# Kernel optimization log

Measured on AMD Instinct MI355X. Metric: run time of the kernel, lower is better.

## Reference

```python
import jax, jax.numpy as jnp
import numpy as np

B, S, D, H = 8, 1024, 1024, 16
HD = D // H  # head_dim = 64


def setup_inputs() -> dict:
    key = jax.random.key(0)
    ks = jax.random.split(key, 5)
    scale = 1.0 / np.sqrt(D)
    return {
        "x": jax.random.normal(ks[0], (B, S, D), dtype=jnp.float32),
        "wq": jax.random.normal(ks[1], (D, D), dtype=jnp.float32) * scale,
        "wk": jax.random.normal(ks[2], (D, D), dtype=jnp.float32) * scale,
        "wv": jax.random.normal(ks[3], (D, D), dtype=jnp.float32) * scale,
        "wo": jax.random.normal(ks[4], (D, D), dtype=jnp.float32) * scale,
    }


def reference(x, wq, wk, wv, wo):
    b, s, d = x.shape
    # nn.Linear: y = x @ W.T  (weights stored [out, in])
    q = (x @ wq.T).reshape(b, s, H, HD).transpose(0, 2, 1, 3)  # [b,h,s,hd]
    k = (x @ wk.T).reshape(b, s, H, HD).transpose(0, 2, 1, 3)
    v = (x @ wv.T).reshape(b, s, H, HD).transpose(0, 2, 1, 3)
    scores = jnp.einsum("bhqd,bhkd->bhqk", q, k) / jnp.sqrt(jnp.float32(HD))
    attn = jax.nn.softmax(scores, axis=-1)  # dropout p=0.0 -> identity
    out = jnp.einsum("bhqk,bhkd->bhqd", attn, v)
    out = out.transpose(0, 2, 1, 3).reshape(b, s, d)
    return out @ wo.T
```

## Files before the change

kernel.cpp:

```cpp
#include <hip/hip_runtime.h>
#include <hip/hip_bf16.h>
#include <math.h>

#define BB 8
#define SS 1024
#define DD 1024
#define HH 16
#define HDIM 64
#define MM (BB * SS)
#define QSCALE 0.1803368801111204f

typedef __attribute__((ext_vector_type(8))) short s8v;
typedef __attribute__((ext_vector_type(4))) short s4v;
typedef __attribute__((ext_vector_type(4))) float f4v;

#define GLD16(g, l)                                                            \
  __builtin_amdgcn_global_load_lds(                                            \
      (const __attribute__((address_space(1))) void*)(g),                      \
      (__attribute__((address_space(3))) void*)(l), 16, 0, 0)

__device__ __forceinline__ unsigned short bf16_ru(float f) {
  return (unsigned short)((__float_as_uint(f) + 0x8000u) >> 16);
}

__global__ void cast_all(const float* __restrict__ x, const float* __restrict__ wq,
                         const float* __restrict__ wk, const float* __restrict__ wv,
                         const float* __restrict__ wo, __hip_bfloat16* __restrict__ xb,
                         __hip_bfloat16* __restrict__ wqkvb,
                         __hip_bfloat16* __restrict__ wob) {
  int blk = blockIdx.x;
  const float* src;
  __hip_bfloat16* dst;
  int base;
  if (blk < 2048) {
    src = x; dst = xb; base = blk * 4096;
  } else if (blk < 2304) {
    src = wq; dst = wqkvb; base = (blk - 2048) * 4096;
  } else if (blk < 2560) {
    src = wk; dst = wqkvb + (1 << 20); base = (blk - 2304) * 4096;
  } else if (blk < 2816) {
    src = wv; dst = wqkvb + (2 << 20); base = (blk - 2560) * 4096;
  } else {
    src = wo; dst = wob; base = (blk - 2816) * 4096;
  }
#pragma unroll
  for (int it = 0; it < 4; ++it) {
    int idx = base + it * 1024 + threadIdx.x * 4;
    float4 f = *(const float4*)&src[idx];
    unsigned short u0 = bf16_ru(f.x), u1 = bf16_ru(f.y);
    unsigned short u2 = bf16_ru(f.z), u3 = bf16_ru(f.w);
    *(uint2*)&dst[idx] = uint2{(unsigned)u0 | ((unsigned)u1 << 16),
                               (unsigned)u2 | ((unsigned)u3 << 16)};
  }
}

template <int MODE>
__global__ __launch_bounds__(256, 2) void gemm_bt(
    const __hip_bfloat16* __restrict__ A, const __hip_bfloat16* __restrict__ Bm,
    float* __restrict__ Cf, __hip_bfloat16* __restrict__ Qo,
    __hip_bfloat16* __restrict__ Ko, __hip_bfloat16* __restrict__ Vt) {
  __shared__ __hip_bfloat16 sA[128 * 32];
  __shared__ __hip_bfloat16 sB[128 * 32];

  const int tid = threadIdx.x;
  const int wave = tid >> 6;
  const int lane = tid & 63;
  const int l15 = lane & 15;
  const int quad = lane >> 4;

  const int m0 = blockIdx.y * 128;
  const int n0 = blockIdx.x * 128;
  const int wm = (wave >> 1) * 64;
  const int wn = (wave & 1) * 64;

  const bool swapT = (MODE == 1) || (n0 < 2048);

  f4v acc[4][4];
#pragma unroll
  for (int i = 0; i < 4; ++i)
#pragma unroll
    for (int j = 0; j < 4; ++j) acc[i][j] = {0.f, 0.f, 0.f, 0.f};

  for (int kt = 0; kt < DD / 32; ++kt) {
    const int k0 = kt * 32;
    __syncthreads();
#pragma unroll
    for (int r = 0; r < 2; ++r) {
      int e = r * 2048 + tid * 8;
      int row = e >> 5, col = e & 31;
      GLD16(A + (size_t)(m0 + row) * DD + k0 + col, &sA[r * 2048 + wave * 512]);
      GLD16(Bm + (size_t)(n0 + row) * DD + k0 + col, &sB[r * 2048 + wave * 512]);
    }
    __syncthreads();

    s8v af[4], bf[4];
#pragma unroll
    for (int i = 0; i < 4; ++i)
      af[i] = *(const s8v*)&sA[(wm + i * 16 + l15) * 32 + quad * 8];
#pragma unroll
    for (int j = 0; j < 4; ++j)
      bf[j] = *(const s8v*)&sB[(wn + j * 16 + l15) * 32 + quad * 8];
    if (swapT) {
#pragma unroll
      for (int i = 0; i < 4; ++i)
#pragma unroll
        for (int j = 0; j < 4; ++j)
          acc[i][j] =
              __builtin_amdgcn_mfma_f32_16x16x32_bf16(bf[j], af[i], acc[i][j], 0, 0, 0);
    } else {
#pragma unroll
      for (int i = 0; i < 4; ++i)
#pragma unroll
        for (int j = 0; j < 4; ++j)
          acc[i][j] =
              __builtin_amdgcn_mfma_f32_16x16x32_bf16(af[i], bf[j], acc[i][j], 0, 0, 0);
    }
  }

#pragma unroll
  for (int i = 0; i < 4; ++i) {
#pragma unroll
    for (int j = 0; j < 4; ++j) {
      if (swapT) {
        const int s_abs = m0 + wm + i * 16 + l15;
        const int col = n0 + wn + j * 16 + quad * 4;
        if (MODE == 0) {
          int which = col >> 10, hcol = col & 1023;
          int h = hcol >> 6, hd = hcol & 63;
          int b = s_abs >> 10, s = s_abs & 1023;
          float scl = (which == 0) ? QSCALE : 1.0f;
          unsigned short us[4];
#pragma unroll
          for (int rg = 0; rg < 4; ++rg) us[rg] = bf16_ru(acc[i][j][rg] * scl);
          __hip_bfloat16* dst = (which == 0) ? Qo : Ko;
          *(uint2*)&dst[((size_t)(b * HH + h) * SS + s) * HDIM + hd] =
              uint2{(unsigned)us[0] | ((unsigned)us[1] << 16),
                    (unsigned)us[2] | ((unsigned)us[3] << 16)};
        } else {
          float4 f4 = {acc[i][j][0], acc[i][j][1], acc[i][j][2], acc[i][j][3]};
          *(float4*)&Cf[(size_t)s_abs * DD + col] = f4;
        }
      } else {
        const int rowb = m0 + wm + i * 16 + quad * 4;
        const int colb = n0 + wn + j * 16 + l15;
        int hcol = colb & 1023;
        int h = hcol >> 6, hd = hcol & 63;
        int b = rowb >> 10, s = rowb & 1023;
        unsigned short us[4];
#pragma unroll
        for (int rg = 0; rg < 4; ++rg) us[rg] = bf16_ru(acc[i][j][rg]);
        *(uint2*)&Vt[((size_t)(b * HH + h) * HDIM + hd) * SS + s] =
            uint2{(unsigned)us[0] | ((unsigned)us[1] << 16),
                  (unsigned)us[2] | ((unsigned)us[3] << 16)};
      }
    }
  }
}

#define KPLD 76
__global__ __launch_bounds__(256, 4) void attn_kernel(
    const __hip_bfloat16* __restrict__ Q, const __hip_bfloat16* __restrict__ K,
    const __hip_bfloat16* __restrict__ Vt, __hip_bfloat16* __restrict__ Oout) {
  __shared__ __hip_bfloat16 sK[64 * 64];
  __shared__ __hip_bfloat16 sVt[64 * 64];
  __shared__ unsigned short sP[4 * 32 * KPLD];

  const int tid = threadIdx.x;
  const int wave = tid >> 6;
  const int lane = tid & 63;
  const int l15 = lane & 15;
  const int quad = lane >> 4;
  const int c8 = lane & 7;
  const int r8 = lane >> 3;

  const int bh = blockIdx.x;
  const int q0 = blockIdx.y * 128;
  const size_t head = (size_t)bh * SS * HDIM;

  unsigned short* sPw = &sP[wave * 32 * KPLD];

  s8v qf[2][2];
#pragma unroll
  for (int mf = 0; mf < 2; ++mf) {
    int s = q0 + wave * 32 + mf * 16 + l15;
#pragma unroll
    for (int kk = 0; kk < 2; ++kk)
      qf[mf][kk] = *(const s8v*)&Q[head + (size_t)s * HDIM + kk * 32 + quad * 8];
  }

  s8v onesB;
#pragma unroll
  for (int j = 0; j < 8; ++j) onesB[j] = (short)0x3F80;

  f4v o[2][4];
  f4v lacc[2];
#pragma unroll
  for (int mf = 0; mf < 2; ++mf) {
    lacc[mf] = {0.f, 0.f, 0.f, 0.f};
#pragma unroll
    for (int f = 0; f < 4; ++f) o[mf][f] = {0.f, 0.f, 0.f, 0.f};
  }

  for (int kb = 0; kb < SS / 64; ++kb) {
    __syncthreads();
#pragma unroll
    for (int r = 0; r < 2; ++r) {
      int rb = r * 32 + wave * 8;
      int row = rb + r8;
      int sc8 = (c8 ^ (row & 7)) * 8;
      GLD16(&K[head + (size_t)(kb * 64 + row) * HDIM + sc8], &sK[rb * 64]);
      GLD16(&Vt[head + (size_t)row * SS + kb * 64 + sc8], &sVt[rb * 64]);
    }
    __syncthreads();

    f4v sc[2][4];
#pragma unroll
    for (int mf = 0; mf < 2; ++mf)
#pragma unroll
      for (int f = 0; f < 4; ++f) sc[mf][f] = {0.f, 0.f, 0.f, 0.f};
#pragma unroll
    for (int kk = 0; kk < 2; ++kk) {
#pragma unroll
      for (int f = 0; f < 4; ++f) {
        s8v kf = *(const s8v*)&sK[(f * 16 + l15) * 64 +
                                  (((kk * 4 + quad) ^ (l15 & 7)) * 8)];
#pragma unroll
        for (int mf = 0; mf < 2; ++mf)
          sc[mf][f] =
              __builtin_amdgcn_mfma_f32_16x16x32_bf16(kf, qf[mf][kk], sc[mf][f], 0, 0, 0);
      }
    }

#pragma unroll
    for (int mf = 0; mf < 2; ++mf)
#pragma unroll
      for (int f = 0; f < 4; ++f) {
        unsigned short us[4];
#pragma unroll
        for (int r = 0; r < 4; ++r) us[r] = bf16_ru(exp2f(sc[mf][f][r]));
        *(uint2*)&sPw[(mf * 16 + l15) * KPLD + f * 16 + quad * 4] =
            uint2{(unsigned)us[0] | ((unsigned)us[1] << 16),
                  (unsigned)us[2] | ((unsigned)us[3] << 16)};
      }

#pragma unroll
    for (int kk = 0; kk < 2; ++kk) {
      s8v pf[2];
#pragma unroll
      for (int mf = 0; mf < 2; ++mf) {
        const unsigned short* p = &sPw[(mf * 16 + l15) * KPLD + kk * 32 + quad * 8];
        s4v lo = *(const s4v*)p;
        s4v hi = *(const s4v*)(p + 4);
        pf[mf] = __builtin_shufflevector(lo, hi, 0, 1, 2, 3, 4, 5, 6, 7);
        lacc[mf] = __builtin_amdgcn_mfma_f32_16x16x32_bf16(pf[mf], onesB, lacc[mf], 0, 0, 0);
      }
#pragma unroll
      for (int f = 0; f < 4; ++f) {
        s8v vf = *(const s8v*)&sVt[(f * 16 + l15) * 64 +
                                   (((kk * 4 + quad) ^ (l15 & 7)) * 8)];
#pragma unroll
        for (int mf = 0; mf < 2; ++mf)
          o[mf][f] =
              __builtin_amdgcn_mfma_f32_16x16x32_bf16(pf[mf], vf, o[mf][f], 0, 0, 0);
      }
    }
  }

  const int b = bh >> 4, h = bh & 15;
#pragma unroll
  for (int mf = 0; mf < 2; ++mf) {
    float rl[4];
#pragma unroll
    for (int r = 0; r < 4; ++r) rl[r] = 1.0f / lacc[mf][r];
#pragma unroll
    for (int f = 0; f < 4; ++f)
#pragma unroll
      for (int r = 0; r < 4; ++r) {
        int srow = q0 + wave * 32 + mf * 16 + quad * 4 + r;
        int col = h * HDIM + f * 16 + l15;
        ((unsigned short*)Oout)[(size_t)(b * SS + srow) * DD + col] =
            bf16_ru(o[mf][f][r] * rl[r]);
      }
  }
}

extern "C" void kernel_launch(void* const* d_in, const int* in_sizes, int n_in,
                              void* d_out, int out_size, void* d_ws, size_t ws_size,
                              hipStream_t stream) {
  const float* x = (const float*)d_in[0];
  const float* wq = (const float*)d_in[1];
  const float* wk = (const float*)d_in[2];
  const float* wv = (const float*)d_in[3];
  const float* wo = (const float*)d_in[4];

  char* ws = (char*)d_ws;
  __hip_bfloat16* xb = (__hip_bfloat16*)(ws);
  __hip_bfloat16* wqkvb = (__hip_bfloat16*)(ws + (16 << 20));
  __hip_bfloat16* wob = (__hip_bfloat16*)(ws + (22 << 20));
  __hip_bfloat16* qh = (__hip_bfloat16*)(ws + (24 << 20));
  __hip_bfloat16* kh = (__hip_bfloat16*)(ws + (40 << 20));
  __hip_bfloat16* vt = (__hip_bfloat16*)(ws + (56 << 20));
  __hip_bfloat16* attnO = (__hip_bfloat16*)(ws + (72 << 20));

  cast_all<<<3072, 256, 0, stream>>>(x, wq, wk, wv, wo, xb, wqkvb, wob);

  gemm_bt<0><<<dim3(24, 64), 256, 0, stream>>>(xb, wqkvb, nullptr, qh, kh, vt);

  attn_kernel<<<dim3(BB * HH, SS / 128), 256, 0, stream>>>(qh, kh, vt, attnO);

  gemm_bt<1><<<dim3(8, 64), 256, 0, stream>>>(attnO, wob, (float*)d_out, nullptr,
                                              nullptr, nullptr);
}
```

Before: 256.0 us.

## Double GEMM K-tile to 64 with XOR-swizzled LDS and split V projection

```diff
diff --git a/kernel.cpp b/kernel.cpp
--- a/kernel.cpp
+++ b/kernel.cpp
@@ -55,65 +55,65 @@
 }
 
 template <int MODE>
-__global__ __launch_bounds__(256, 2) void gemm_bt(
+__global__ __launch_bounds__(256, 3) void gemm_bt(
     const __hip_bfloat16* __restrict__ A, const __hip_bfloat16* __restrict__ Bm,
     float* __restrict__ Cf, __hip_bfloat16* __restrict__ Qo,
     __hip_bfloat16* __restrict__ Ko, __hip_bfloat16* __restrict__ Vt) {
-  __shared__ __hip_bfloat16 sA[128 * 32];
-  __shared__ __hip_bfloat16 sB[128 * 32];
+  __shared__ __hip_bfloat16 sA[128 * 64];
+  __shared__ __hip_bfloat16 sB[128 * 64];
 
   const int tid = threadIdx.x;
   const int wave = tid >> 6;
   const int lane = tid & 63;
   const int l15 = lane & 15;
   const int quad = lane >> 4;
+  const int c8 = lane & 7;
+  const int r8 = lane >> 3;
 
   const int m0 = blockIdx.y * 128;
   const int n0 = blockIdx.x * 128;
   const int wm = (wave >> 1) * 64;
   const int wn = (wave & 1) * 64;
 
-  const bool swapT = (MODE == 1) || (n0 < 2048);
-
   f4v acc[4][4];
 #pragma unroll
   for (int i = 0; i < 4; ++i)
 #pragma unroll
     for (int j = 0; j < 4; ++j) acc[i][j] = {0.f, 0.f, 0.f, 0.f};
 
-  for (int kt = 0; kt < DD / 32; ++kt) {
-    const int k0 = kt * 32;
+  for (int kt = 0; kt < DD / 64; ++kt) {
+    const int k0 = kt * 64;
     __syncthreads();
 #pragma unroll
-    for (int r = 0; r < 2; ++r) {
-      int e = r * 2048 + tid * 8;
-      int row = e >> 5, col = e & 31;
-      GLD16(A + (size_t)(m0 + row) * DD + k0 + col, &sA[r * 2048 + wave * 512]);
-      GLD16(Bm + (size_t)(n0 + row) * DD + k0 + col, &sB[r * 2048 + wave * 512]);
+    for (int r = 0; r < 4; ++r) {
+      int rb = r * 32 + wave * 8;
+      int row = rb + r8;
+      int scol = (c8 ^ (row & 7)) * 8;
+      GLD16(A + (size_t)(m0 + row) * DD + k0 + scol, &sA[rb * 64]);
+      GLD16(Bm + (size_t)(n0 + row) * DD + k0 + scol, &sB[rb * 64]);
     }
     __syncthreads();
 
-    s8v af[4], bf[4];
-#pragma unroll
-    for (int i = 0; i < 4; ++i)
-      af[i] = *(const s8v*)&sA[(wm + i * 16 + l15) * 32 + quad * 8];
-#pragma unroll
-    for (int j = 0; j < 4; ++j)
-      bf[j] = *(const s8v*)&sB[(wn + j * 16 + l15) * 32 + quad * 8];
-    if (swapT) {
+#pragma unroll
+    for (int kk = 0; kk < 2; ++kk) {
+      s8v af[4], bf[4];
 #pragma unroll
       for (int i = 0; i < 4; ++i)
+        af[i] = *(const s8v*)&sA[(wm + i * 16 + l15) * 64 +
+                                 (((kk * 4 + quad) ^ (l15 & 7)) * 8)];
+#pragma unroll
+      for (int j = 0; j < 4; ++j)
+        bf[j] = *(const s8v*)&sB[(wn + j * 16 + l15) * 64 +
+                                 (((kk * 4 + quad) ^ (l15 & 7)) * 8)];
+#pragma unroll
+      for (int i = 0; i < 4; ++i)
 #pragma unroll
         for (int j = 0; j < 4; ++j)
-          acc[i][j] =
-              __builtin_amdgcn_mfma_f32_16x16x32_bf16(bf[j], af[i], acc[i][j], 0, 0, 0);
-    } else {
-#pragma unroll
-      for (int i = 0; i < 4; ++i)
-#pragma unroll
-        for (int j = 0; j < 4; ++j)
-          acc[i][j] =
-              __builtin_amdgcn_mfma_f32_16x16x32_bf16(af[i], bf[j], acc[i][j], 0, 0, 0);
+          acc[i][j] = (MODE == 2)
+                          ? __builtin_amdgcn_mfma_f32_16x16x32_bf16(af[i], bf[j],
+                                                                    acc[i][j], 0, 0, 0)
+                          : __builtin_amdgcn_mfma_f32_16x16x32_bf16(bf[j], af[i],
+                                                                    acc[i][j], 0, 0, 0);
     }
   }
 
@@ -121,31 +121,31 @@
   for (int i = 0; i < 4; ++i) {
 #pragma unroll
     for (int j = 0; j < 4; ++j) {
-      if (swapT) {
+      if (MODE == 0) {
         const int s_abs = m0 + wm + i * 16 + l15;
         const int col = n0 + wn + j * 16 + quad * 4;
-        if (MODE == 0) {
-          int which = col >> 10, hcol = col & 1023;
-          int h = hcol >> 6, hd = hcol & 63;
-          int b = s_abs >> 10, s = s_abs & 1023;
-          float scl = (which == 0) ? QSCALE : 1.0f;
-          unsigned short us[4];
-#pragma unroll
-          for (int rg = 0; rg < 4; ++rg) us[rg] = bf16_ru(acc[i][j][rg] * scl);
-          __hip_bfloat16* dst = (which == 0) ? Qo : Ko;
-          *(uint2*)&dst[((size_t)(b * HH + h) * SS + s) * HDIM + hd] =
-              uint2{(unsigned)us[0] | ((unsigned)us[1] << 16),
-                    (unsigned)us[2] | ((unsigned)us[3] << 16)};
-        } else {
-          float4 f4 = {acc[i][j][0], acc[i][j][1], acc[i][j][2], acc[i][j][3]};
-          *(float4*)&Cf[(size_t)s_abs * DD + col] = f4;
-        }
+        const bool isQ = (n0 < 1024);
+        const int hcol = col & 1023;
+        const int h = hcol >> 6, hd = hcol & 63;
+        const int b = s_abs >> 10, s = s_abs & 1023;
+        const float scl = isQ ? QSCALE : 1.0f;
+        __hip_bfloat16* dst = isQ ? Qo : Ko;
+        unsigned short us[4];
+#pragma unroll
+        for (int rg = 0; rg < 4; ++rg) us[rg] = bf16_ru(acc[i][j][rg] * scl);
+        *(uint2*)&dst[((size_t)(b * HH + h) * SS + s) * HDIM + hd] =
+            uint2{(unsigned)us[0] | ((unsigned)us[1] << 16),
+                  (unsigned)us[2] | ((unsigned)us[3] << 16)};
+      } else if (MODE == 1) {
+        const int s_abs = m0 + wm + i * 16 + l15;
+        const int col = n0 + wn + j * 16 + quad * 4;
+        float4 f4 = {acc[i][j][0], acc[i][j][1], acc[i][j][2], acc[i][j][3]};
+        *(float4*)&Cf[(size_t)s_abs * DD + col] = f4;
       } else {
         const int rowb = m0 + wm + i * 16 + quad * 4;
         const int colb = n0 + wn + j * 16 + l15;
-        int hcol = colb & 1023;
-        int h = hcol >> 6, hd = hcol & 63;
-        int b = rowb >> 10, s = rowb & 1023;
+        const int h = colb >> 6, hd = colb & 63;
+        const int b = rowb >> 10, s = rowb & 1023;
         unsigned short us[4];
 #pragma unroll
         for (int rg = 0; rg < 4; ++rg) us[rg] = bf16_ru(acc[i][j][rg]);
@@ -304,7 +304,9 @@
 
   cast_all<<<3072, 256, 0, stream>>>(x, wq, wk, wv, wo, xb, wqkvb, wob);
 
-  gemm_bt<0><<<dim3(24, 64), 256, 0, stream>>>(xb, wqkvb, nullptr, qh, kh, vt);
+  gemm_bt<0><<<dim3(16, 64), 256, 0, stream>>>(xb, wqkvb, nullptr, qh, kh, nullptr);
+  gemm_bt<2><<<dim3(8, 64), 256, 0, stream>>>(xb, wqkvb + (2 << 20), nullptr,
+                                              nullptr, nullptr, vt);
 
   attn_kernel<<<dim3(BB * HH, SS / 128), 256, 0, stream>>>(qh, kh, vt, attnO);
 
```

New measurement: 239.1 us. -6.6%, faster.
